# Kernel tuning notes

Hardware: AMD Instinct MI355X
Metric: run time of the kernel (lower is better)

## Reference

```python
import jax, jax.numpy as jnp
import numpy as np

B, H, S, D = 4, 16, 2048, 128

def setup_inputs() -> dict:
    key = jax.random.key(0)
    k1, k2 = jax.random.split(key)
    x2 = jax.random.normal(k1, (B, H, S, D), dtype=jnp.float32)
    x3 = jax.random.normal(k2, (B, H, S, D), dtype=jnp.float32)
    return {"x2": x2, "x3": x3}

def reference(x2, x3):
    # scores: [B,H,S,S] = x2 @ x3^T (unscaled)
    scores = jnp.einsum('bhqd,bhkd->bhqk', x2, x3)
    probs = jax.nn.softmax(scores, axis=-1)
    # output: [B,H,S,D] = probs @ x3
    return jnp.einsum('bhqk,bhkd->bhqd', probs, x3)
```

## Files before the change

kernel.cpp:

```cpp
#include <hip/hip_runtime.h>
#include <hip/hip_bf16.h>

typedef __attribute__((ext_vector_type(4))) float f32x4;
typedef _Float16 f16;
typedef __attribute__((ext_vector_type(8))) _Float16 f16x8;
typedef __attribute__((ext_vector_type(4))) _Float16 f16x4;
typedef __attribute__((ext_vector_type(2))) __fp16 pk16x2;
typedef __attribute__((ext_vector_type(2))) unsigned int uint2v;

#define S_LEN 2048
#define D_DIM 128
#define QBLK 128
#define KVBLK 64
#define NKV (S_LEN / KVBLK)

__device__ __forceinline__ float hired_max(float x) {
    uint2v s = __builtin_amdgcn_permlane16_swap(__float_as_uint(x), __float_as_uint(x), false, false);
    float m = fmaxf(__uint_as_float(s.x), __uint_as_float(s.y));
    uint2v s2 = __builtin_amdgcn_permlane32_swap(__float_as_uint(m), __float_as_uint(m), false, false);
    return fmaxf(__uint_as_float(s2.x), __uint_as_float(s2.y));
}
__device__ __forceinline__ float hired_sum(float x) {
    uint2v s = __builtin_amdgcn_permlane16_swap(__float_as_uint(x), __float_as_uint(x), false, false);
    float m = __uint_as_float(s.x) + __uint_as_float(s.y);
    uint2v s2 = __builtin_amdgcn_permlane32_swap(__float_as_uint(m), __float_as_uint(m), false, false);
    return __uint_as_float(s2.x) + __uint_as_float(s2.y);
}

__global__ __launch_bounds__(256, 2) void attn_kernel(
    const float* __restrict__ Q, const float* __restrict__ KV,
    float* __restrict__ Out)
{
    unsigned b = blockIdx.x;
    unsigned cpx = gridDim.x >> 3;
    unsigned work = (b & 7u) * cpx + (b >> 3);
    unsigned head = work >> 4;
    unsigned qt = work & 15u;

    const float* Qh = Q + (size_t)head * (S_LEN * D_DIM) + (size_t)qt * QBLK * D_DIM;
    const float* Kh = KV + (size_t)head * (S_LEN * D_DIM);
    float* Oh = Out + (size_t)head * (S_LEN * D_DIM) + (size_t)qt * QBLK * D_DIM;

    const int tid = threadIdx.x;
    const int wv = tid >> 6;
    const int lane = tid & 63;
    const int lo = lane & 15;
    const int hi = lane >> 4;

    __shared__ __align__(16) f16 Ksh[KVBLK * D_DIM];
    __shared__ __align__(16) f16 Vsh[D_DIM * KVBLK];

    const int srow = (tid >> 5) * 8;
    const int scol = (tid & 31) * 4;

    f16x8 qf[2][4];
    #pragma unroll
    for (int t = 0; t < 2; ++t) {
        const float* qr = Qh + (wv * 32 + t * 16 + lo) * D_DIM + hi * 8;
        #pragma unroll
        for (int kc = 0; kc < 4; ++kc) {
            f32x4 a = *(const f32x4*)(qr + kc * 32);
            f32x4 c = *(const f32x4*)(qr + kc * 32 + 4);
            pk16x2 p0 = __builtin_amdgcn_cvt_pkrtz(a[0], a[1]);
            pk16x2 p1 = __builtin_amdgcn_cvt_pkrtz(a[2], a[3]);
            pk16x2 p2 = __builtin_amdgcn_cvt_pkrtz(c[0], c[1]);
            pk16x2 p3 = __builtin_amdgcn_cvt_pkrtz(c[2], c[3]);
            f16x8 q;
            q[0] = (f16)p0[0]; q[1] = (f16)p0[1]; q[2] = (f16)p1[0]; q[3] = (f16)p1[1];
            q[4] = (f16)p2[0]; q[5] = (f16)p2[1]; q[6] = (f16)p3[0]; q[7] = (f16)p3[1];
            qf[t][kc] = q;
        }
    }

    f32x4 oacc[2][8];
    #pragma unroll
    for (int t = 0; t < 2; ++t)
        #pragma unroll
        for (int n = 0; n < 8; ++n) oacc[t][n] = (f32x4){0.f, 0.f, 0.f, 0.f};
    float mr[2] = {-1e30f, -1e30f};
    float lr[2] = {0.f, 0.f};

    f32x4 stg[8];

    #define STAGE_LOAD(KT) do {                                               \
        const float* p_ = Kh + (size_t)(KT) * KVBLK * D_DIM + srow * D_DIM + scol; \
        _Pragma("unroll")                                                     \
        for (int i_ = 0; i_ < 8; ++i_) stg[i_] = *(const f32x4*)(p_ + i_ * D_DIM); \
    } while (0)

    #define STAGE_WRITE() do {                                                \
        _Pragma("unroll")                                                     \
        for (int i_ = 0; i_ < 8; ++i_) {                                      \
            int row_ = srow + i_;                                             \
            int fK_ = (row_ & 7) ^ ((row_ >> 3) & 7);                         \
            pk16x2 a_ = __builtin_amdgcn_cvt_pkrtz(stg[i_][0], stg[i_][1]);   \
            pk16x2 b_ = __builtin_amdgcn_cvt_pkrtz(stg[i_][2], stg[i_][3]);   \
            f16x4 w_;                                                         \
            w_[0] = (f16)a_[0]; w_[1] = (f16)a_[1];                           \
            w_[2] = (f16)b_[0]; w_[3] = (f16)b_[1];                           \
            *(f16x4*)&Ksh[row_ * D_DIM + (scol ^ (fK_ << 3))] = w_;           \
        }                                                                     \
        _Pragma("unroll")                                                     \
        for (int j_ = 0; j_ < 4; ++j_) {                                      \
            int d_ = scol + j_;                                               \
            int g_ = (d_ & 7) ^ ((d_ >> 3) & 7);                              \
            pk16x2 a0_ = __builtin_amdgcn_cvt_pkrtz(stg[0][j_], stg[1][j_]);  \
            pk16x2 a1_ = __builtin_amdgcn_cvt_pkrtz(stg[2][j_], stg[3][j_]);  \
            pk16x2 a2_ = __builtin_amdgcn_cvt_pkrtz(stg[4][j_], stg[5][j_]);  \
            pk16x2 a3_ = __builtin_amdgcn_cvt_pkrtz(stg[6][j_], stg[7][j_]);  \
            f16x8 w_;                                                         \
            w_[0] = (f16)a0_[0]; w_[1] = (f16)a0_[1];                         \
            w_[2] = (f16)a1_[0]; w_[3] = (f16)a1_[1];                         \
            w_[4] = (f16)a2_[0]; w_[5] = (f16)a2_[1];                         \
            w_[6] = (f16)a3_[0]; w_[7] = (f16)a3_[1];                         \
            *(f16x8*)&Vsh[d_ * KVBLK + (srow ^ (g_ << 3))] = w_;              \
        }                                                                     \
    } while (0)

    STAGE_LOAD(0);
    STAGE_WRITE();
    __syncthreads();

    for (int kt = 0; kt < NKV; ++kt) {
        if (kt + 1 < NKV) STAGE_LOAD(kt + 1);

        f32x4 st[2][4];
        #pragma unroll
        for (int t = 0; t < 2; ++t)
            #pragma unroll
            for (int m = 0; m < 4; ++m) st[t][m] = (f32x4){0.f, 0.f, 0.f, 0.f};
        __builtin_amdgcn_s_setprio(1);
        #pragma unroll
        for (int m = 0; m < 4; ++m) {
            int row = m * 16 + lo;
            int fK = (row & 7) ^ ((row >> 3) & 7);
            #pragma unroll
            for (int kc = 0; kc < 4; ++kc) {
                f16x8 kf = *(const f16x8*)&Ksh[row * D_DIM + ((kc * 32 + hi * 8) ^ (fK << 3))];
                st[0][m] = __builtin_amdgcn_mfma_f32_16x16x32_f16(kf, qf[0][kc], st[0][m], 0, 0, 0);
                st[1][m] = __builtin_amdgcn_mfma_f32_16x16x32_f16(kf, qf[1][kc], st[1][m], 0, 0, 0);
            }
        }
        __builtin_amdgcn_s_setprio(0);

        f16x8 pf[2][2];
        #pragma unroll
        for (int t = 0; t < 2; ++t) {
            float tmax = -1e30f;
            #pragma unroll
            for (int m = 0; m < 4; ++m)
                #pragma unroll
                for (int r = 0; r < 4; ++r) tmax = fmaxf(tmax, st[t][m][r]);
            tmax = hired_max(tmax);

            bool skip = __all(tmax - mr[t] <= 8.0f);
            float mnew = skip ? mr[t] : fmaxf(mr[t], tmax);

            float ls = 0.f;
            #pragma unroll
            for (int m = 0; m < 4; ++m) {
                #pragma unroll
                for (int r = 0; r < 4; ++r) {
                    float p = __expf(st[t][m][r] - mnew);
                    st[t][m][r] = p;
                    ls += p;
                }
            }
            ls = hired_sum(ls);

            if (!skip) {
                float scale = __expf(mr[t] - mnew);
                lr[t] = lr[t] * scale + ls;
                float sc4[4];
                #pragma unroll
                for (int r = 0; r < 4; ++r) sc4[r] = __shfl(scale, hi * 4 + r, 64);
                #pragma unroll
                for (int n = 0; n < 8; ++n)
                    #pragma unroll
                    for (int r = 0; r < 4; ++r) oacc[t][n][r] *= sc4[r];
                mr[t] = mnew;
            } else {
                lr[t] += ls;
            }

            unsigned cc[4][2];
            #pragma unroll
            for (int m = 0; m < 4; ++m) {
                union { pk16x2 p; unsigned u; } ua, ub;
                ua.p = __builtin_amdgcn_cvt_pkrtz(st[t][m][0], st[t][m][1]);
                ub.p = __builtin_amdgcn_cvt_pkrtz(st[t][m][2], st[t][m][3]);
                cc[m][0] = ua.u; cc[m][1] = ub.u;
            }
            #pragma unroll
            for (int kc2 = 0; kc2 < 2; ++kc2) {
                unsigned r0 = cc[2 * kc2][0], r1 = cc[2 * kc2][1];
                unsigned r2 = cc[2 * kc2 + 1][0], r3 = cc[2 * kc2 + 1][1];
                uint2v s02 = __builtin_amdgcn_permlane32_swap(r0, r2, false, false);
                uint2v s13 = __builtin_amdgcn_permlane32_swap(r1, r3, false, false);
                uint2v t02 = __builtin_amdgcn_permlane16_swap(s02.x, s02.y, false, false);
                uint2v t13 = __builtin_amdgcn_permlane16_swap(s13.x, s13.y, false, false);
                union { unsigned u[4]; f16x8 v; } pu;
                pu.u[0] = t02.x; pu.u[1] = t13.x; pu.u[2] = t02.y; pu.u[3] = t13.y;
                pf[t][kc2] = pu.v;
            }
        }

        __builtin_amdgcn_s_setprio(1);
        #pragma unroll
        for (int kc2 = 0; kc2 < 2; ++kc2) {
            #pragma unroll
            for (int n = 0; n < 8; ++n) {
                int d = n * 16 + lo;
                int g = (d & 7) ^ ((d >> 3) & 7);
                f16x8 vf = *(const f16x8*)&Vsh[d * KVBLK + ((kc2 * 32 + hi * 8) ^ (g << 3))];
                oacc[0][n] = __builtin_amdgcn_mfma_f32_16x16x32_f16(pf[0][kc2], vf, oacc[0][n], 0, 0, 0);
                oacc[1][n] = __builtin_amdgcn_mfma_f32_16x16x32_f16(pf[1][kc2], vf, oacc[1][n], 0, 0, 0);
            }
        }
        __builtin_amdgcn_s_setprio(0);

        __syncthreads();
        if (kt + 1 < NKV) {
            STAGE_WRITE();
            __syncthreads();
        }
    }

    #pragma unroll
    for (int t = 0; t < 2; ++t) {
        float inv = 1.0f / lr[t];
        float rl[4];
        #pragma unroll
        for (int r = 0; r < 4; ++r) rl[r] = __shfl(inv, hi * 4 + r, 64);
        #pragma unroll
        for (int n = 0; n < 8; ++n)
            #pragma unroll
            for (int r = 0; r < 4; ++r)
                Oh[(wv * 32 + t * 16 + hi * 4 + r) * D_DIM + n * 16 + lo] = oacc[t][n][r] * rl[r];
    }
}

extern "C" void kernel_launch(void* const* d_in, const int* in_sizes, int n_in,
                              void* d_out, int out_size, void* d_ws, size_t ws_size,
                              hipStream_t stream) {
    const float* x2 = (const float*)d_in[0];
    const float* x3 = (const float*)d_in[1];
    float* out = (float*)d_out;
    dim3 grid(1024), block(256);
    hipLaunchKernelGGL(attn_kernel, grid, block, 0, stream, x2, x3, out);
}
```

Baseline: 170.0 us.

## Fold log2e into Q, use exp2, split QK per row-tile, raise occupancy

```diff
diff --git a/kernel.cpp b/kernel.cpp
--- a/kernel.cpp
+++ b/kernel.cpp
@@ -13,6 +13,9 @@
 #define QBLK 128
 #define KVBLK 64
 #define NKV (S_LEN / KVBLK)
+#define LOG2E 1.44269504088896340736f
+
+#define EXP2(x) __builtin_amdgcn_exp2f(x)
 
 __device__ __forceinline__ float hired_max(float x) {
     uint2v s = __builtin_amdgcn_permlane16_swap(__float_as_uint(x), __float_as_uint(x), false, false);
@@ -27,7 +30,7 @@
     return __uint_as_float(s2.x) + __uint_as_float(s2.y);
 }
 
-__global__ __launch_bounds__(256, 2) void attn_kernel(
+__global__ __launch_bounds__(256, 3) void attn_kernel(
     const float* __restrict__ Q, const float* __restrict__ KV,
     float* __restrict__ Out)
 {
@@ -61,10 +64,10 @@
         for (int kc = 0; kc < 4; ++kc) {
             f32x4 a = *(const f32x4*)(qr + kc * 32);
             f32x4 c = *(const f32x4*)(qr + kc * 32 + 4);
-            pk16x2 p0 = __builtin_amdgcn_cvt_pkrtz(a[0], a[1]);
-            pk16x2 p1 = __builtin_amdgcn_cvt_pkrtz(a[2], a[3]);
-            pk16x2 p2 = __builtin_amdgcn_cvt_pkrtz(c[0], c[1]);
-            pk16x2 p3 = __builtin_amdgcn_cvt_pkrtz(c[2], c[3]);
+            pk16x2 p0 = __builtin_amdgcn_cvt_pkrtz(a[0] * LOG2E, a[1] * LOG2E);
+            pk16x2 p1 = __builtin_amdgcn_cvt_pkrtz(a[2] * LOG2E, a[3] * LOG2E);
+            pk16x2 p2 = __builtin_amdgcn_cvt_pkrtz(c[0] * LOG2E, c[1] * LOG2E);
+            pk16x2 p3 = __builtin_amdgcn_cvt_pkrtz(c[2] * LOG2E, c[3] * LOG2E);
             f16x8 q;
             q[0] = (f16)p0[0]; q[1] = (f16)p0[1]; q[2] = (f16)p1[0]; q[3] = (f16)p1[1];
             q[4] = (f16)p2[0]; q[5] = (f16)p2[1]; q[6] = (f16)p3[0]; q[7] = (f16)p3[1];
@@ -124,36 +127,33 @@
     for (int kt = 0; kt < NKV; ++kt) {
         if (kt + 1 < NKV) STAGE_LOAD(kt + 1);
 
-        f32x4 st[2][4];
-        #pragma unroll
-        for (int t = 0; t < 2; ++t)
-            #pragma unroll
-            for (int m = 0; m < 4; ++m) st[t][m] = (f32x4){0.f, 0.f, 0.f, 0.f};
-        __builtin_amdgcn_s_setprio(1);
-        #pragma unroll
-        for (int m = 0; m < 4; ++m) {
-            int row = m * 16 + lo;
-            int fK = (row & 7) ^ ((row >> 3) & 7);
-            #pragma unroll
-            for (int kc = 0; kc < 4; ++kc) {
-                f16x8 kf = *(const f16x8*)&Ksh[row * D_DIM + ((kc * 32 + hi * 8) ^ (fK << 3))];
-                st[0][m] = __builtin_amdgcn_mfma_f32_16x16x32_f16(kf, qf[0][kc], st[0][m], 0, 0, 0);
-                st[1][m] = __builtin_amdgcn_mfma_f32_16x16x32_f16(kf, qf[1][kc], st[1][m], 0, 0, 0);
-            }
-        }
-        __builtin_amdgcn_s_setprio(0);
-
         f16x8 pf[2][2];
         #pragma unroll
         for (int t = 0; t < 2; ++t) {
+            f32x4 st[4];
+            #pragma unroll
+            for (int m = 0; m < 4; ++m) st[m] = (f32x4){0.f, 0.f, 0.f, 0.f};
+            __builtin_amdgcn_s_setprio(1);
+            #pragma unroll
+            for (int m = 0; m < 4; ++m) {
+                int row = m * 16 + lo;
+                int fK = (row & 7) ^ ((row >> 3) & 7);
+                #pragma unroll
+                for (int kc = 0; kc < 4; ++kc) {
+                    f16x8 kf = *(const f16x8*)&Ksh[row * D_DIM + ((kc * 32 + hi * 8) ^ (fK << 3))];
+                    st[m] = __builtin_amdgcn_mfma_f32_16x16x32_f16(kf, qf[t][kc], st[m], 0, 0, 0);
+                }
+            }
+            __builtin_amdgcn_s_setprio(0);
+
             float tmax = -1e30f;
             #pragma unroll
             for (int m = 0; m < 4; ++m)
                 #pragma unroll
-                for (int r = 0; r < 4; ++r) tmax = fmaxf(tmax, st[t][m][r]);
+                for (int r = 0; r < 4; ++r) tmax = fmaxf(tmax, st[m][r]);
             tmax = hired_max(tmax);
 
-            bool skip = __all(tmax - mr[t] <= 8.0f);
+            bool skip = __all(tmax - mr[t] <= 11.5415603f);
             float mnew = skip ? mr[t] : fmaxf(mr[t], tmax);
 
             float ls = 0.f;
@@ -161,15 +161,15 @@
             for (int m = 0; m < 4; ++m) {
                 #pragma unroll
                 for (int r = 0; r < 4; ++r) {
-                    float p = __expf(st[t][m][r] - mnew);
-                    st[t][m][r] = p;
+                    float p = EXP2(st[m][r] - mnew);
+                    st[m][r] = p;
                     ls += p;
                 }
             }
             ls = hired_sum(ls);
 
             if (!skip) {
-                float scale = __expf(mr[t] - mnew);
+                float scale = EXP2(mr[t] - mnew);
                 lr[t] = lr[t] * scale + ls;
                 float sc4[4];
                 #pragma unroll
@@ -187,8 +187,8 @@
             #pragma unroll
             for (int m = 0; m < 4; ++m) {
                 union { pk16x2 p; unsigned u; } ua, ub;
-                ua.p = __builtin_amdgcn_cvt_pkrtz(st[t][m][0], st[t][m][1]);
-                ub.p = __builtin_amdgcn_cvt_pkrtz(st[t][m][2], st[t][m][3]);
+                ua.p = __builtin_amdgcn_cvt_pkrtz(st[m][0], st[m][1]);
+                ub.p = __builtin_amdgcn_cvt_pkrtz(st[m][2], st[m][3]);
                 cc[m][0] = ua.u; cc[m][1] = ub.u;
             }
             #pragma unroll
```

Measured after the change: 607.1 us. 257% more time.
